# Performance work log

Measured on AMD Instinct MI355X. Metric: run time of the kernel, lower is better.

## Reference

```python
import jax, jax.numpy as jnp
import numpy as np
from jax import lax

DIM = 2048
HEAD_DIM = 128
N_HEADS = 16
N_KV_HEADS = 4
N_REP = N_HEADS // N_KV_HEADS
K_CHUNK = 8          # token_chunk
SEQ = 2048
BATCH = 1
ROPE_THETA = 10000.0
KV_DIM = N_KV_HEADS * HEAD_DIM  # 512


def _make_freq_cis(seq, hd, theta):
    # (seq, hd//2, 2, 2) rotation matrices [[cos, -sin], [sin, cos]]
    inv = 1.0 / (theta ** (np.arange(0, hd, 2, dtype=np.float64) / hd))
    ang = np.outer(np.arange(seq, dtype=np.float64), inv)
    cos, sin = np.cos(ang), np.sin(ang)
    f = np.stack([np.stack([cos, -sin], -1), np.stack([sin, cos], -1)], -2)
    return jnp.asarray(f, jnp.float32)


def setup_inputs() -> dict:
    key = jax.random.key(0)
    ks = jax.random.split(key, 12)
    s = 0.02
    inp = {
        'x': jax.random.normal(ks[0], (BATCH, SEQ, DIM), jnp.float32),
        'freq_cis': _make_freq_cis(SEQ, HEAD_DIM, ROPE_THETA),
        # nn.Linear weights stored as (out, in); y = x @ W.T
        'wq': jax.random.normal(ks[1], (N_HEADS * HEAD_DIM, DIM), jnp.float32) * s,
        'wk': jax.random.normal(ks[2], (KV_DIM, DIM), jnp.float32) * s,
        'wv': jax.random.normal(ks[3], (KV_DIM, DIM), jnp.float32) * s,
        'wo': jax.random.normal(ks[4], (DIM, N_HEADS * HEAD_DIM), jnp.float32) * s,
        # diagonal SSM params for k_ssm / v_ssm (per-channel)
        'a_log_k': jax.random.normal(ks[5], (KV_DIM,), jnp.float32) * 0.5,
        'b_k': jax.random.normal(ks[6], (KV_DIM,), jnp.float32),
        'c_k': jax.random.normal(ks[7], (KV_DIM,), jnp.float32),
        'a_log_v': jax.random.normal(ks[8], (KV_DIM,), jnp.float32) * 0.5,
        'b_v': jax.random.normal(ks[9], (KV_DIM,), jnp.float32),
        'c_v': jax.random.normal(ks[10], (KV_DIM,), jnp.float32),
    }
    return inp


def _ssm_chunked(x, a_log, b, c):
    # Chunked diagonal SSM with state reset every K_CHUNK tokens
    # (equivalent to flat_process_chunks_with_ssm with boundaries every K).
    bsz, S, E = x.shape
    nc = S // K_CHUNK
    a = jnp.exp(-jax.nn.softplus(a_log))  # (E,) decay in (0, 1)
    xs = x.reshape(bsz * nc, K_CHUNK, E).swapaxes(0, 1)  # (K, N, E)

    def step(h, xt):
        h = a * h + b * xt
        return h, c * h

    _, ys = lax.scan(step, jnp.zeros((bsz * nc, E), x.dtype), xs)
    return ys.swapaxes(0, 1).reshape(bsz, S, E)


def _apply_rope(xq, xk, freq_cis):
    # xq: (b, s, h, hd); freq_cis: (s, hd//2, 2, 2)
    def rot(t):
        b, s, h, hd = t.shape
        tr = t.reshape(b, s, h, hd // 2, 1, 2)
        f = freq_cis.reshape(1, s, 1, hd // 2, 2, 2)
        return (tr * f).sum(-1).reshape(b, s, h, hd)
    return rot(xq), rot(xk)


def _forward(x, freq_cis, wq, wk, wv, wo, a_log_k, b_k, c_k, a_log_v, b_v, c_v):
    bsz, S, _ = x.shape
    xq = jnp.einsum('bsd,ed->bse', x, wq)
    xk = jnp.einsum('bsd,ed->bse', x, wk)
    xv = jnp.einsum('bsd,ed->bse', x, wv)

    # chunked SSM preprocessing of K/V (+ residual_ssm)
    xk_p = _ssm_chunked(xk, a_log_k, b_k, c_k) + xk
    xv_p = _ssm_chunked(xv, a_log_v, b_v, c_v) + xv

    xq = xq.reshape(bsz, S, N_HEADS, HEAD_DIM)
    xk_p = xk_p.reshape(bsz, S, N_KV_HEADS, HEAD_DIM)
    xv_p = xv_p.reshape(bsz, S, N_KV_HEADS, HEAD_DIM)

    xq, xk_p = _apply_rope(xq, xk_p, freq_cis)

    # GQA repeat_kv (torch.repeat_interleave on head dim)
    xk_p = jnp.repeat(xk_p, N_REP, axis=2)
    xv_p = jnp.repeat(xv_p, N_REP, axis=2)

    # chunk-boundary attention mask
    k_pos = jnp.arange(S)
    boundary = (k_pos % K_CHUNK) == (K_CHUNK - 1)
    t = jnp.arange(S)[:, None]
    k = k_pos[None, :]
    mask = ((k < t) & boundary[None, :]) | (k == t - 1) | ((k < 4) & (k <= t))

    q = xq.transpose(0, 2, 1, 3)   # (b, h, s, d)
    kk = xk_p.transpose(0, 2, 1, 3)
    vv = xv_p.transpose(0, 2, 1, 3)

    scores = jnp.einsum('bhqd,bhkd->bhqk', q, kk) / jnp.sqrt(
        jnp.asarray(HEAD_DIM, q.dtype))
    scores = jnp.where(mask[None, None], scores, -jnp.inf)
    attn = jax.nn.softmax(scores, axis=-1)
    out = jnp.einsum('bhqk,bhkd->bhqd', attn, vv)
    out = out.transpose(0, 2, 1, 3).reshape(bsz, S, N_HEADS * HEAD_DIM)
    return jnp.einsum('bse,de->bsd', out, wo)


def reference(x, freq_cis, wq, wk, wv, wo, a_log_k, b_k, c_k,
              a_log_v, b_v, c_v):
    return _forward(x, freq_cis, wq, wk, wv, wo,
                    a_log_k, b_k, c_k, a_log_v, b_v, c_v)
```

## Files before the change

### kernel.cpp

```cpp
#include <hip/hip_runtime.h>

typedef __bf16 bf16x8 __attribute__((ext_vector_type(8)));
typedef float  f32x4  __attribute__((ext_vector_type(4)));
typedef unsigned short u16;
typedef unsigned int   u32;

__device__ __forceinline__ float b2f(u16 u) {
    u32 x = ((u32)u) << 16;
    return __builtin_bit_cast(float, x);
}
__device__ __forceinline__ u16 f2b(float f) {
    u32 x = __builtin_bit_cast(u32, f);
    x += 0x7fffu + ((x >> 16) & 1u);
    return (u16)(x >> 16);
}

__global__ void convert_kernel(const float* __restrict__ x, const float* __restrict__ wq,
                               const float* __restrict__ wk, const float* __restrict__ wv,
                               const float* __restrict__ wo,
                               u16* __restrict__ xb, u16* __restrict__ wcat, u16* __restrict__ wob)
{
    long i4 = (long)blockIdx.x * 256 + threadIdx.x;
    long e = i4 * 4;
    const float* src; u16* dst;
    if (e < 4194304) { src = x + e; dst = xb + e; }
    else if (e < 10485760) {
        long j = e - 4194304;
        dst = wcat + j;
        if (j < 4194304)      src = wq + j;
        else if (j < 5242880) src = wk + (j - 4194304);
        else                  src = wv + (j - 5242880);
    } else {
        long j = e - 10485760;
        src = wo + j; dst = wob + j;
    }
    float4 v = *(const float4*)src;
    uint2 pk;
    pk.x = (u32)f2b(v.x) | ((u32)f2b(v.y) << 16);
    pk.y = (u32)f2b(v.z) | ((u32)f2b(v.w) << 16);
    *(uint2*)dst = pk;
}

template<int OUT_BF16>
__global__ __launch_bounds__(256) void gemm_bt_kernel(
    const u16* __restrict__ A, const u16* __restrict__ B,
    void* __restrict__ Cout, int M, int N, int K)
{
    __shared__ u16 As[2][8192];
    __shared__ u16 Bs[2][4096];
    const int tid  = threadIdx.x;
    const int lane = tid & 63;
    const int wave = tid >> 6;
    const int waveM = wave >> 1, waveN = wave & 1;
    const int tm = blockIdx.y * 128;
    const int tn = blockIdx.x * 64;

    f32x4 acc[4][2];
#pragma unroll
    for (int i = 0; i < 4; ++i)
#pragma unroll
        for (int j = 0; j < 2; ++j) acc[i][j] = f32x4{0.f, 0.f, 0.f, 0.f};

    const int frow = lane & 15;
    const int fk   = (lane >> 4) * 8;

    auto STAGE = [&](int buf, int kt) {
#pragma unroll
        for (int c = 0; c < 4; ++c) {
            int idx = c * 256 + tid;
            int row = idx >> 3;
            int blk = (idx & 7) ^ (row & 7);
            const u16* srcA = A + (size_t)(tm + row) * K + kt + blk * 8;
            u16* dstA = &As[buf][(size_t)(c * 256 + wave * 64) * 8];
            __builtin_amdgcn_global_load_lds((const __attribute__((address_space(1))) void*)srcA,
                                             (__attribute__((address_space(3))) void*)dstA, 16, 0, 0);
        }
#pragma unroll
        for (int c = 0; c < 2; ++c) {
            int idx = c * 256 + tid;
            int row = idx >> 3;
            int blk = (idx & 7) ^ (row & 7);
            const u16* srcB = B + (size_t)(tn + row) * K + kt + blk * 8;
            u16* dstB = &Bs[buf][(size_t)(c * 256 + wave * 64) * 8];
            __builtin_amdgcn_global_load_lds((const __attribute__((address_space(1))) void*)srcB,
                                             (__attribute__((address_space(3))) void*)dstB, 16, 0, 0);
        }
    };
    auto COMPUTE = [&](int buf) {
#pragma unroll
        for (int kk = 0; kk < 64; kk += 32) {
            bf16x8 af[4], bfr[2];
#pragma unroll
            for (int m = 0; m < 4; ++m) {
                int r  = waveM * 64 + m * 16 + frow;
                int kb_ = ((kk + fk) >> 3) ^ (r & 7);
                af[m] = *(const bf16x8*)&As[buf][r * 64 + kb_ * 8];
            }
#pragma unroll
            for (int n = 0; n < 2; ++n) {
                int r  = waveN * 32 + n * 16 + frow;
                int kb_ = ((kk + fk) >> 3) ^ (r & 7);
                bfr[n] = *(const bf16x8*)&Bs[buf][r * 64 + kb_ * 8];
            }
#pragma unroll
            for (int m = 0; m < 4; ++m)
#pragma unroll
                for (int n = 0; n < 2; ++n)
                    acc[m][n] = __builtin_amdgcn_mfma_f32_16x16x32_bf16(af[m], bfr[n], acc[m][n], 0, 0, 0);
        }
    };

    const int nk = K >> 6;
    STAGE(0, 0);
    int buf = 0;
    for (int t = 0; t < nk - 1; ++t) {
        STAGE(buf ^ 1, (t + 1) << 6);
        asm volatile("s_waitcnt vmcnt(6)" ::: "memory");
        __builtin_amdgcn_s_barrier();
        __builtin_amdgcn_sched_barrier(0);
        COMPUTE(buf);
        __builtin_amdgcn_sched_barrier(0);
        __builtin_amdgcn_s_barrier();
        buf ^= 1;
    }
    asm volatile("s_waitcnt vmcnt(0)" ::: "memory");
    __builtin_amdgcn_s_barrier();
    __builtin_amdgcn_sched_barrier(0);
    COMPUTE(buf);

    const int rb = tm + waveM * 64;
    const int cb = tn + waveN * 32;
#pragma unroll
    for (int m = 0; m < 4; ++m)
#pragma unroll
        for (int n = 0; n < 2; ++n)
#pragma unroll
            for (int r = 0; r < 4; ++r) {
                int row = rb + m * 16 + (lane >> 4) * 4 + r;
                int col = cb + n * 16 + (lane & 15);
                if (OUT_BF16) ((u16*)Cout)[(size_t)row * N + col] = f2b(acc[m][n][r]);
                else          ((float*)Cout)[(size_t)row * N + col] = acc[m][n][r];
            }
}

__global__ void ssm_rope_kernel(const u16* __restrict__ c1, const float* __restrict__ fc,
                                const float* __restrict__ alk, const float* __restrict__ bk,
                                const float* __restrict__ ck,
                                const float* __restrict__ alv, const float* __restrict__ bv,
                                const float* __restrict__ cv,
                                u16* __restrict__ qb, u16* __restrict__ kb, u16* __restrict__ vb)
{
    int gi = blockIdx.x * 256 + threadIdx.x;
    if (gi < 2097152) {
        int s = gi >> 10, pg = gi & 1023;
        int i = pg & 63;
        int e0 = (pg >> 6) * 128 + 2 * i;
        u32 u = *(const u32*)&c1[(size_t)s * 3072 + e0];
        float x0 = b2f((u16)(u & 0xffff)), x1 = b2f((u16)(u >> 16));
        float4 f = *(const float4*)&fc[((size_t)s * 64 + i) * 4];
        float q0 = x0 * f.x - x1 * f.z;
        float q1 = x0 * f.z + x1 * f.x;
        *(u32*)&qb[(size_t)s * 2048 + e0] = (u32)f2b(q0) | ((u32)f2b(q1) << 16);
    } else if (gi < 2097152 + 65536) {
        int ki = gi - 2097152;
        int chunk = ki >> 8, pr = ki & 255;
        int i = pr & 63;
        int e0 = (pr >> 6) * 128 + 2 * i;
        float z0 = alk[e0], z1 = alk[e0 + 1];
        float sp0 = z0 > 20.f ? z0 : log1pf(__expf(z0));
        float sp1 = z1 > 20.f ? z1 : log1pf(__expf(z1));
        float a0 = __expf(-sp0), a1 = __expf(-sp1);
        float b0 = bk[e0], b1 = bk[e0 + 1];
        float c0 = ck[e0], cc1 = ck[e0 + 1];
        float h0 = 0.f, h1 = 0.f;
#pragma unroll
        for (int tt = 0; tt < 8; ++tt) {
            int s = chunk * 8 + tt;
            u32 u = *(const u32*)&c1[(size_t)s * 3072 + 2048 + e0];
            float x0 = b2f((u16)(u & 0xffff)), x1 = b2f((u16)(u >> 16));
            h0 = a0 * h0 + b0 * x0;
            h1 = a1 * h1 + b1 * x1;
            float y0 = c0 * h0 + x0;
            float y1 = cc1 * h1 + x1;
            float4 f = *(const float4*)&fc[((size_t)s * 64 + i) * 4];
            float k0 = y0 * f.x - y1 * f.z;
            float k1 = y0 * f.z + y1 * f.x;
            *(u32*)&kb[(size_t)s * 512 + e0] = (u32)f2b(k0) | ((u32)f2b(k1) << 16);
        }
    } else {
        int vi = gi - 2097152 - 65536;
        int chunk = vi >> 9, e = vi & 511;
        float z = alv[e];
        float sp = z > 20.f ? z : log1pf(__expf(z));
        float a = __expf(-sp);
        float b = bv[e], c = cv[e];
        float h = 0.f;
#pragma unroll
        for (int tt = 0; tt < 8; ++tt) {
            int s = chunk * 8 + tt;
            float xvv = b2f(c1[(size_t)s * 3072 + 2560 + e]);
            h = a * h + b * xvv;
            vb[(size_t)s * 512 + e] = f2b(c * h + xvv);
        }
    }
}

__global__ void compact_kernel(const u16* __restrict__ kb, const u16* __restrict__ vb,
                               u16* __restrict__ kbc, u16* __restrict__ vbt)
{
    int id = blockIdx.x * 256 + threadIdx.x;
    int kvh = id >> 15, rem = id & 32767, j = rem >> 7, d = rem & 127;
    int src = (8 * j + 7) * 512 + kvh * 128 + d;
    kbc[(((kvh << 8) + j) << 7) + d] = kb[src];
    vbt[(((kvh << 7) + d) << 8) + j] = vb[src];
}

__global__ __launch_bounds__(512, 2) void attn_kernel(
    const u16* __restrict__ qb, const u16* __restrict__ kb, const u16* __restrict__ vb,
    const u16* __restrict__ kbc, const u16* __restrict__ vbt, u16* __restrict__ aout)
{
    __shared__ u16   ksbuf[32768];
    __shared__ u16   vsbuf[32768];
    __shared__ float p_ext[8][16][32];

    const int tid  = threadIdx.x;
    const int w    = tid >> 6;
    const int lane = tid & 63;
    const int s    = lane & 15;
    const int g    = lane >> 4;
    const int h    = blockIdx.x >> 4;
    const int t0   = (blockIdx.x & 15) * 128;
    const int kvh  = h >> 2;
    const int qw   = t0 + w * 16;

    {
        const u16* kcb = kbc + ((size_t)kvh << 15);
#pragma unroll
        for (int it = 0; it < 8; ++it) {
            int idx = it * 512 + tid;
            int r = idx >> 4, b = idx & 15;
            const u16* src = kcb + r * 128 + ((b ^ (r & 7)) << 3);
            u16* dst = ksbuf + (size_t)(it * 512 + w * 64) * 8;
            __builtin_amdgcn_global_load_lds((const __attribute__((address_space(1))) void*)src,
                                             (__attribute__((address_space(3))) void*)dst, 16, 0, 0);
        }
    }
    __syncthreads();

    {
        const u16* vtb = vbt + ((size_t)kvh << 15);
#pragma unroll
        for (int it = 0; it < 8; ++it) {
            int idx = it * 512 + tid;
            int r = idx >> 5, b = idx & 31;
            const u16* src = vtb + r * 256 + ((b ^ (r & 7)) << 3);
            u16* dst = vsbuf + (size_t)(it * 512 + w * 64) * 8;
            __builtin_amdgcn_global_load_lds((const __attribute__((address_space(1))) void*)src,
                                             (__attribute__((address_space(3))) void*)dst, 16, 0, 0);
        }
    }

    bf16x8 qa[4];
    {
        const u16* qr = qb + (size_t)(qw + s) * 2048 + h * 128 + g * 8;
#pragma unroll
        for (int kk = 0; kk < 4; ++kk) qa[kk] = *(const bf16x8*)&qr[kk * 32];
    }

    f32x4 sf[18];
#pragma unroll
    for (int i = 0; i < 18; ++i) sf[i] = f32x4{0.f, 0.f, 0.f, 0.f};

#pragma unroll
    for (int fb = 0; fb < 16; ++fb) {
        int row = fb * 16 + s;
#pragma unroll
        for (int kk = 0; kk < 4; ++kk) {
            int ch = (kk * 4 + g) ^ (s & 7);
            bf16x8 bf = *(const bf16x8*)&ksbuf[row * 128 + ch * 8];
            sf[fb] = __builtin_amdgcn_mfma_f32_16x16x32_bf16(qa[kk], bf, sf[fb], 0, 0, 0);
        }
    }
#pragma unroll
    for (int xb = 0; xb < 2; ++xb) {
        int i = xb * 16 + s;
        int keyrow = (i < 4) ? i : (qw + (i - 4) - 1);
        if (keyrow < 0) keyrow = 0;
        if (keyrow > 2047) keyrow = 2047;
        const u16* kr = kb + (size_t)keyrow * 512 + kvh * 128 + g * 8;
#pragma unroll
        for (int kk = 0; kk < 4; ++kk) {
            bf16x8 bf = *(const bf16x8*)&kr[kk * 32];
            sf[16 + xb] = __builtin_amdgcn_mfma_f32_16x16x32_bf16(qa[kk], bf, sf[16 + xb], 0, 0, 0);
        }
    }

    const float scale = 0.08838834764831845f;
    float mx[4] = {-1e30f, -1e30f, -1e30f, -1e30f};
#pragma unroll
    for (int fi = 0; fi < 18; ++fi)
#pragma unroll
        for (int r = 0; r < 4; ++r) {
            int q = g * 4 + r;
            int t = qw + q;
            bool ok;
            if (fi < 16) {
                int j = fi * 16 + s;
                ok = j < (t >> 3);
            } else {
                int i = (fi - 16) * 16 + s;
                if (i < 4) ok = (i <= t);
                else       ok = ((i - 4) == q) && ((t & 7) != 0) && (t >= 5);
            }
            float v = ok ? sf[fi][r] * scale : -1e30f;
            sf[fi][r] = v;
            mx[r] = fmaxf(mx[r], v);
        }
#pragma unroll
    for (int r = 0; r < 4; ++r)
#pragma unroll
        for (int off = 8; off; off >>= 1) mx[r] = fmaxf(mx[r], __shfl_xor(mx[r], off));

    float sm[4] = {0.f, 0.f, 0.f, 0.f};
#pragma unroll
    for (int fi = 0; fi < 18; ++fi)
#pragma unroll
        for (int r = 0; r < 4; ++r) {
            float p = __expf(sf[fi][r] - mx[r]);
            sf[fi][r] = p;
            sm[r] += p;
        }
#pragma unroll
    for (int r = 0; r < 4; ++r)
#pragma unroll
        for (int off = 8; off; off >>= 1) sm[r] += __shfl_xor(sm[r], off);
    float inv[4];
#pragma unroll
    for (int r = 0; r < 4; ++r) inv[r] = 1.f / sm[r];

    __syncthreads();

    u16* pbuf = ksbuf + w * 4096;
#pragma unroll
    for (int fi = 0; fi < 16; ++fi)
#pragma unroll
        for (int r = 0; r < 4; ++r) {
            int q = g * 4 + r;
            int c = fi * 16 + s;
            int blk = (c >> 3) ^ q;
            pbuf[q * 256 + (blk << 3) + (c & 7)] = f2b(sf[fi][r]);
        }
#pragma unroll
    for (int xb = 0; xb < 2; ++xb)
#pragma unroll
        for (int r = 0; r < 4; ++r)
            p_ext[w][g * 4 + r][xb * 16 + s] = sf[16 + xb][r];

    bf16x8 pa[8];
#pragma unroll
    for (int kk = 0; kk < 8; ++kk) {
        int blk = (kk * 4 + g) ^ s;
        pa[kk] = *(const bf16x8*)&pbuf[s * 256 + (blk << 3)];
    }
    f32x4 out[8];
#pragma unroll
    for (int f = 0; f < 8; ++f) out[f] = f32x4{0.f, 0.f, 0.f, 0.f};
#pragma unroll
    for (int f = 0; f < 8; ++f) {
        int row = f * 16 + s;
#pragma unroll
        for (int kk = 0; kk < 8; ++kk) {
            int ch = (kk * 4 + g) ^ (s & 7);
            bf16x8 vf = *(const bf16x8*)&vsbuf[row * 256 + ch * 8];
            out[f] = __builtin_amdgcn_mfma_f32_16x16x32_bf16(pa[kk], vf, out[f], 0, 0, 0);
        }
    }

    {
        float v4[4][8];
#pragma unroll
        for (int e = 0; e < 4; ++e)
#pragma unroll
            for (int f = 0; f < 8; ++f)
                v4[e][f] = b2f(vb[(size_t)e * 512 + kvh * 128 + f * 16 + s]);
#pragma unroll
        for (int r = 0; r < 4; ++r) {
            int q = g * 4 + r;
            int t = qw + q;
#pragma unroll
            for (int e = 0; e < 4; ++e) {
                float p = p_ext[w][q][e];
#pragma unroll
                for (int f = 0; f < 8; ++f) out[f][r] += p * v4[e][f];
            }
            float pp = p_ext[w][q][4 + q];
            int key = t - 1; if (key < 0) key = 0;
            const u16* vr = vb + (size_t)key * 512 + kvh * 128;
#pragma unroll
            for (int f = 0; f < 8; ++f) out[f][r] += pp * b2f(vr[f * 16 + s]);
        }
    }

#pragma unroll
    for (int f = 0; f < 8; ++f)
#pragma unroll
        for (int r = 0; r < 4; ++r) {
            int t = qw + g * 4 + r;
            aout[(size_t)t * 2048 + h * 128 + f * 16 + s] = f2b(out[f][r] * inv[r]);
        }
}

extern "C" void kernel_launch(void* const* d_in, const int* in_sizes, int n_in,
                              void* d_out, int out_size, void* d_ws, size_t ws_size,
                              hipStream_t stream) {
    const float* x   = (const float*)d_in[0];
    const float* fc  = (const float*)d_in[1];
    const float* wq  = (const float*)d_in[2];
    const float* wk  = (const float*)d_in[3];
    const float* wv  = (const float*)d_in[4];
    const float* wo  = (const float*)d_in[5];
    const float* alk = (const float*)d_in[6];
    const float* bk  = (const float*)d_in[7];
    const float* ck  = (const float*)d_in[8];
    const float* alv = (const float*)d_in[9];
    const float* bv  = (const float*)d_in[10];
    const float* cv  = (const float*)d_in[11];

    char* ws = (char*)d_ws;
    u16*   xb   = (u16*)(ws);
    u16*   wcat = (u16*)(ws + 8388608);
    u16*   wob  = (u16*)(ws + 20971520);
    u16*   c1   = (u16*)(ws + 29360128);
    u16*   qb   = (u16*)(ws + 54525952);
    u16*   kb   = (u16*)(ws + 62914560);
    u16*   vb   = (u16*)(ws + 65011712);
    u16*   kbc  = (u16*)(ws + 67108864);
    u16*   vbt  = (u16*)(ws + 67371008);
    u16*   aout = (u16*)(ws + 67633152);

    convert_kernel<<<14336, 256, 0, stream>>>(x, wq, wk, wv, wo, xb, wcat, wob);

    dim3 g1(3072 / 64, 2048 / 128);
    gemm_bt_kernel<1><<<g1, 256, 0, stream>>>(xb, wcat, (void*)c1, 2048, 3072, 2048);

    ssm_rope_kernel<<<8960, 256, 0, stream>>>(c1, fc, alk, bk, ck, alv, bv, cv, qb, kb, vb);

    compact_kernel<<<512, 256, 0, stream>>>(kb, vb, kbc, vbt);

    attn_kernel<<<256, 512, 0, stream>>>(qb, kb, vb, kbc, vbt, aout);

    dim3 g3(2048 / 64, 2048 / 128);
    gemm_bt_kernel<0><<<g3, 256, 0, stream>>>(aout, wob, d_out, 2048, 2048, 2048);
}
```

Before: 111.9 us.

## Fuse Q RoPE into QKV GEMM epilogue and compaction into SSM kernel

The QKV projection GEMM now applies RoPE to the Q columns directly in its epilogue, pairing adjacent columns with a lane shuffle, and writes only the K/V columns to a narrower intermediate. The SSM kernel now also writes the compacted chunk-boundary K and transposed V entries, so the separate compaction kernel is removed. This cuts two kernel launches and a full round trip of the Q intermediate through global memory. In exchange the GEMM epilogue does scattered per-element frequency loads and 16-bit stores.

```diff
diff --git a/kernel.cpp b/kernel.cpp
--- a/kernel.cpp
+++ b/kernel.cpp
@@ -41,10 +41,11 @@
     *(uint2*)dst = pk;
 }
 
-template<int OUT_BF16>
+template<int MODE>
 __global__ __launch_bounds__(256) void gemm_bt_kernel(
     const u16* __restrict__ A, const u16* __restrict__ B,
-    void* __restrict__ Cout, int M, int N, int K)
+    void* __restrict__ Cout, int M, int N, int K,
+    u16* __restrict__ qb, u16* __restrict__ c1kv, const float* __restrict__ fc)
 {
     __shared__ u16 As[2][8192];
     __shared__ u16 Bs[2][4096];
@@ -130,40 +131,61 @@
 
     const int rb = tm + waveM * 64;
     const int cb = tn + waveN * 32;
-#pragma unroll
-    for (int m = 0; m < 4; ++m)
-#pragma unroll
-        for (int n = 0; n < 2; ++n)
-#pragma unroll
-            for (int r = 0; r < 4; ++r) {
-                int row = rb + m * 16 + (lane >> 4) * 4 + r;
-                int col = cb + n * 16 + (lane & 15);
-                if (OUT_BF16) ((u16*)Cout)[(size_t)row * N + col] = f2b(acc[m][n][r]);
-                else          ((float*)Cout)[(size_t)row * N + col] = acc[m][n][r];
-            }
-}
-
-__global__ void ssm_rope_kernel(const u16* __restrict__ c1, const float* __restrict__ fc,
-                                const float* __restrict__ alk, const float* __restrict__ bk,
-                                const float* __restrict__ ck,
-                                const float* __restrict__ alv, const float* __restrict__ bv,
-                                const float* __restrict__ cv,
-                                u16* __restrict__ qb, u16* __restrict__ kb, u16* __restrict__ vb)
+    const int s  = lane & 15;
+    if (MODE == 0) {
+#pragma unroll
+        for (int m = 0; m < 4; ++m)
+#pragma unroll
+            for (int n = 0; n < 2; ++n)
+#pragma unroll
+                for (int r = 0; r < 4; ++r) {
+                    int row = rb + m * 16 + (lane >> 4) * 4 + r;
+                    int col = cb + n * 16 + s;
+                    ((float*)Cout)[(size_t)row * N + col] = acc[m][n][r];
+                }
+    } else if (tn < 2048) {
+#pragma unroll
+        for (int m = 0; m < 4; ++m)
+#pragma unroll
+            for (int n = 0; n < 2; ++n)
+#pragma unroll
+                for (int r = 0; r < 4; ++r) {
+                    int row = rb + m * 16 + (lane >> 4) * 4 + r;
+                    int col = cb + n * 16 + s;
+                    float val  = acc[m][n][r];
+                    float part = __shfl_xor(val, 1);
+                    int i = (col & 127) >> 1;
+                    const float* f4 = &fc[((size_t)row * 64 + i) * 4];
+                    float cs = f4[0], sn = f4[2];
+                    float q = (s & 1) ? (part * sn + val * cs)
+                                      : (val * cs - part * sn);
+                    qb[(size_t)row * 2048 + col] = f2b(q);
+                }
+    } else {
+#pragma unroll
+        for (int m = 0; m < 4; ++m)
+#pragma unroll
+            for (int n = 0; n < 2; ++n)
+#pragma unroll
+                for (int r = 0; r < 4; ++r) {
+                    int row = rb + m * 16 + (lane >> 4) * 4 + r;
+                    int col = cb + n * 16 + s;
+                    c1kv[(size_t)row * 1024 + (col - 2048)] = f2b(acc[m][n][r]);
+                }
+    }
+}
+
+__global__ void ssm_kv_kernel(const u16* __restrict__ c1kv, const float* __restrict__ fc,
+                              const float* __restrict__ alk, const float* __restrict__ bk,
+                              const float* __restrict__ ck,
+                              const float* __restrict__ alv, const float* __restrict__ bv,
+                              const float* __restrict__ cv,
+                              u16* __restrict__ kb, u16* __restrict__ vb,
+                              u16* __restrict__ kbc, u16* __restrict__ vbt)
 {
     int gi = blockIdx.x * 256 + threadIdx.x;
-    if (gi < 2097152) {
-        int s = gi >> 10, pg = gi & 1023;
-        int i = pg & 63;
-        int e0 = (pg >> 6) * 128 + 2 * i;
-        u32 u = *(const u32*)&c1[(size_t)s * 3072 + e0];
-        float x0 = b2f((u16)(u & 0xffff)), x1 = b2f((u16)(u >> 16));
-        float4 f = *(const float4*)&fc[((size_t)s * 64 + i) * 4];
-        float q0 = x0 * f.x - x1 * f.z;
-        float q1 = x0 * f.z + x1 * f.x;
-        *(u32*)&qb[(size_t)s * 2048 + e0] = (u32)f2b(q0) | ((u32)f2b(q1) << 16);
-    } else if (gi < 2097152 + 65536) {
-        int ki = gi - 2097152;
-        int chunk = ki >> 8, pr = ki & 255;
+    if (gi < 65536) {
+        int chunk = gi >> 8, pr = gi & 255;
         int i = pr & 63;
         int e0 = (pr >> 6) * 128 + 2 * i;
         float z0 = alk[e0], z1 = alk[e0 + 1];
@@ -173,22 +195,26 @@
         float b0 = bk[e0], b1 = bk[e0 + 1];
         float c0 = ck[e0], cc1 = ck[e0 + 1];
         float h0 = 0.f, h1 = 0.f;
+        int kvh = e0 >> 7, d = e0 & 127;
 #pragma unroll
         for (int tt = 0; tt < 8; ++tt) {
-            int s = chunk * 8 + tt;
-            u32 u = *(const u32*)&c1[(size_t)s * 3072 + 2048 + e0];
+            int sr = chunk * 8 + tt;
+            u32 u = *(const u32*)&c1kv[(size_t)sr * 1024 + e0];
             float x0 = b2f((u16)(u & 0xffff)), x1 = b2f((u16)(u >> 16));
             h0 = a0 * h0 + b0 * x0;
             h1 = a1 * h1 + b1 * x1;
             float y0 = c0 * h0 + x0;
             float y1 = cc1 * h1 + x1;
-            float4 f = *(const float4*)&fc[((size_t)s * 64 + i) * 4];
-            float k0 = y0 * f.x - y1 * f.z;
-            float k1 = y0 * f.z + y1 * f.x;
-            *(u32*)&kb[(size_t)s * 512 + e0] = (u32)f2b(k0) | ((u32)f2b(k1) << 16);
+            const float* f4 = &fc[((size_t)sr * 64 + i) * 4];
+            float k0 = y0 * f4[0] - y1 * f4[2];
+            float k1 = y0 * f4[2] + y1 * f4[0];
+            u32 pk = (u32)f2b(k0) | ((u32)f2b(k1) << 16);
+            *(u32*)&kb[(size_t)sr * 512 + e0] = pk;
+            if (tt == 7)
+                *(u32*)&kbc[(size_t)kvh * 32768 + chunk * 128 + d] = pk;
         }
     } else {
-        int vi = gi - 2097152 - 65536;
+        int vi = gi - 65536;
         int chunk = vi >> 9, e = vi & 511;
         float z = alv[e];
         float sp = z > 20.f ? z : log1pf(__expf(z));
@@ -197,22 +223,15 @@
         float h = 0.f;
 #pragma unroll
         for (int tt = 0; tt < 8; ++tt) {
-            int s = chunk * 8 + tt;
-            float xvv = b2f(c1[(size_t)s * 3072 + 2560 + e]);
+            int sr = chunk * 8 + tt;
+            float xvv = b2f(c1kv[(size_t)sr * 1024 + 512 + e]);
             h = a * h + b * xvv;
-            vb[(size_t)s * 512 + e] = f2b(c * h + xvv);
-        }
-    }
-}
-
-__global__ void compact_kernel(const u16* __restrict__ kb, const u16* __restrict__ vb,
-                               u16* __restrict__ kbc, u16* __restrict__ vbt)
-{
-    int id = blockIdx.x * 256 + threadIdx.x;
-    int kvh = id >> 15, rem = id & 32767, j = rem >> 7, d = rem & 127;
-    int src = (8 * j + 7) * 512 + kvh * 128 + d;
-    kbc[(((kvh << 8) + j) << 7) + d] = kb[src];
-    vbt[(((kvh << 7) + d) << 8) + j] = vb[src];
+            u16 y = f2b(c * h + xvv);
+            vb[(size_t)sr * 512 + e] = y;
+            if (tt == 7)
+                vbt[((size_t)e << 8) + chunk] = y;
+        }
+    }
 }
 
 __global__ __launch_bounds__(512, 2) void attn_kernel(
@@ -430,7 +449,7 @@
     u16*   xb   = (u16*)(ws);
     u16*   wcat = (u16*)(ws + 8388608);
     u16*   wob  = (u16*)(ws + 20971520);
-    u16*   c1   = (u16*)(ws + 29360128);
+    u16*   c1kv = (u16*)(ws + 29360128);
     u16*   qb   = (u16*)(ws + 54525952);
     u16*   kb   = (u16*)(ws + 62914560);
     u16*   vb   = (u16*)(ws + 65011712);
@@ -441,14 +460,15 @@
     convert_kernel<<<14336, 256, 0, stream>>>(x, wq, wk, wv, wo, xb, wcat, wob);
 
     dim3 g1(3072 / 64, 2048 / 128);
-    gemm_bt_kernel<1><<<g1, 256, 0, stream>>>(xb, wcat, (void*)c1, 2048, 3072, 2048);
-
-    ssm_rope_kernel<<<8960, 256, 0, stream>>>(c1, fc, alk, bk, ck, alv, bv, cv, qb, kb, vb);
-
-    compact_kernel<<<512, 256, 0, stream>>>(kb, vb, kbc, vbt);
+    gemm_bt_kernel<1><<<g1, 256, 0, stream>>>(xb, wcat, nullptr, 2048, 3072, 2048,
+                                              qb, c1kv, fc);
+
+    ssm_kv_kernel<<<768, 256, 0, stream>>>(c1kv, fc, alk, bk, ck, alv, bv, cv,
+                                           kb, vb, kbc, vbt);
 
     attn_kernel<<<256, 512, 0, stream>>>(qb, kb, vb, kbc, vbt, aout);
 
     dim3 g3(2048 / 64, 2048 / 128);
-    gemm_bt_kernel<0><<<g3, 256, 0, stream>>>(aout, wob, d_out, 2048, 2048, 2048);
-}
+    gemm_bt_kernel<0><<<g3, 256, 0, stream>>>(aout, wob, d_out, 2048, 2048, 2048,
+                                              nullptr, nullptr, nullptr);
+}
```

New measurement: 102.4 us (median of 2 runs). 1.09x faster.
